# Optimization experiments

Hardware: AMD Instinct MI355X
Metric: run time of the kernel (lower is better)

The kernel has to match this reference:

```python
import jax, jax.numpy as jnp
import numpy as np

SEQ, BATCH, IN, HID, MID = 512, 64, 64, 512, 256


def setup_inputs() -> dict:
    key = jax.random.key(0)
    ks = jax.random.split(key, 8)
    concat_size = IN + 2 * HID  # 1088
    z_size = IN + MID  # 320
    sc = lambda n: 1.0 / np.sqrt(n)
    return {
        "x": jax.random.normal(ks[0], (SEQ, BATCH, IN), dtype=jnp.float32),
        "old_m": jax.random.normal(ks[1], (BATCH, HID), dtype=jnp.float32),
        "old_s": jnp.ones((BATCH, HID), dtype=jnp.float32),
        "W_z": jax.random.normal(ks[2], (MID, concat_size), dtype=jnp.float32) * sc(concat_size),
        "b_z": jnp.zeros((MID,), dtype=jnp.float32),
        "W_s": jax.random.normal(ks[3], (HID, z_size), dtype=jnp.float32) * sc(z_size),
        "b_s": jnp.zeros((HID,), dtype=jnp.float32),
        "W_m": jax.random.normal(ks[4], (HID, z_size), dtype=jnp.float32) * sc(z_size),
        "b_m": jnp.zeros((HID,), dtype=jnp.float32),
    }


def reference(x, old_m, old_s, W_z, b_z, W_s, b_s, W_m, b_m):
    def step(carry, x_t):
        m, s = carry  # [B, H] each
        z_inpt = jnp.concatenate([x_t, m, 1.0 / s], axis=-1)  # [B, IN+2H]
        z = jnp.concatenate([x_t, jnp.tanh(z_inpt @ W_z.T + b_z)], axis=-1)  # [B, IN+MID]
        new_s = s + jax.nn.sigmoid(z @ W_s.T + b_s)
        m_gate = jax.lax.stop_gradient(s / new_s)
        new_m = m_gate * m + (1.0 - m_gate) * jnp.tanh(z @ W_m.T + b_m)
        return (new_m, new_s), (new_m, new_s)

    _, (out_m, out_s) = jax.lax.scan(step, (old_m, old_s), x)
    return out_m, out_s
```

## Files before the change

### kernel.cpp

```cpp
#include <hip/hip_runtime.h>
#include <math.h>
#include <stdint.h>

#define SEQ    512
#define BATCH  64
#define IN_    64
#define HID    512
#define MID    256
#define CONCAT 1088
#define ZS     320
#define NW     4
#define QZ     64

typedef _Float16 h2t __attribute__((ext_vector_type(2)));

__device__ __forceinline__ float fdot2u(uint32_t a, uint32_t b, float c) {
    return __builtin_amdgcn_fdot2(__builtin_bit_cast(h2t, a),
                                  __builtin_bit_cast(h2t, b), c, false);
}
__device__ __forceinline__ uint32_t packrtn(float a, float b) {
    h2t h = { (_Float16)a, (_Float16)b };
    return __builtin_bit_cast(uint32_t, h);
}
template <int CTRL>
__device__ __forceinline__ float dpp_add(float v) {
    int o = __builtin_amdgcn_update_dpp(0, __builtin_bit_cast(int, v), CTRL, 0xF, 0xF, true);
    return v + __builtin_bit_cast(float, o);
}
template <int CTRL>
__device__ __forceinline__ float dpp_get(float v) {
    int o = __builtin_amdgcn_update_dpp(0, __builtin_bit_cast(int, v), CTRL, 0xF, 0xF, true);
    return __builtin_bit_cast(float, o);
}
__device__ __forceinline__ float red16(float v) {
    v = dpp_add<0xB1>(v);
    v = dpp_add<0x4E>(v);
    v = dpp_add<0x124>(v);
    v = dpp_add<0x128>(v);
    return v;
}
__device__ __forceinline__ int zidx(int k) { return (k / 34) * 36 + (k % 34); }

__device__ uint64_t g_px[(size_t)BATCH * 2 * NW * HID];

__global__ __launch_bounds__(512, 1)
void metamu8_kernel(const float* __restrict__ x,
                    const float* __restrict__ old_m,
                    const float* __restrict__ old_s,
                    const float* __restrict__ W_z,
                    const float* __restrict__ b_z,
                    const float* __restrict__ W_s,
                    const float* __restrict__ b_s,
                    const float* __restrict__ W_m,
                    const float* __restrict__ b_m,
                    float* __restrict__ out)
{
    const int bid = blockIdx.x;
    const int b   = bid & 63;
    const int w   = bid >> 6;
    const int tid = threadIdx.x;
    const int h   = tid;

    __shared__ __align__(16) uint32_t zin2[2][16 * 36];
    __shared__ __align__(16) uint32_t zvec2[2][40];

    const int g = tid >> 4, c = tid & 15;

    uint32_t wA0[34], wA1[34];
    {
        const float* p0 = W_z + (size_t)(QZ * w + 2 * g) * CONCAT + 68 * c;
        const float* p1 = p0 + CONCAT;
        #pragma unroll
        for (int i = 0; i < 34; ++i) {
            float2 a  = *reinterpret_cast<const float2*>(p0 + 2 * i);
            float2 bb = *reinterpret_cast<const float2*>(p1 + 2 * i);
            wA0[i] = packrtn(a.x, a.y);
            wA1[i] = packrtn(bb.x, bb.y);
        }
    }
    uint32_t wS[40], wM[40];
    {
        const float* ps = W_s + (size_t)h * ZS;
        const float* pm = W_m + (size_t)h * ZS;
        #pragma unroll
        for (int i = 0; i < 8; ++i) {
            float2 a  = *reinterpret_cast<const float2*>(ps + 16 * w + 2 * i);
            float2 bb = *reinterpret_cast<const float2*>(pm + 16 * w + 2 * i);
            wS[i] = packrtn(a.x, a.y);
            wM[i] = packrtn(bb.x, bb.y);
        }
        #pragma unroll
        for (int i = 0; i < 32; ++i) {
            float2 a  = *reinterpret_cast<const float2*>(ps + 64 + 64 * w + 2 * i);
            float2 bb = *reinterpret_cast<const float2*>(pm + 64 + 64 * w + 2 * i);
            wS[8 + i] = packrtn(a.x, a.y);
            wM[8 + i] = packrtn(bb.x, bb.y);
        }
    }
    const float bz0 = b_z[QZ * w + 2 * g], bz1 = b_z[QZ * w + 2 * g + 1];
    const float bsv = b_s[h], bmv = b_m[h];

    float sreg = old_s[b * HID + h];
    float mreg = old_m[b * HID + h];

    float2 xv = {0.f, 0.f};
    if (tid < 32) xv = *reinterpret_cast<const float2*>(x + (size_t)b * IN_ + 2 * tid);

    if (tid < 256) {
        float2 mv = *reinterpret_cast<const float2*>(old_m + b * HID + 2 * tid);
        zin2[0][zidx(32 + tid)] = packrtn(mv.x, mv.y);
    } else {
        const int j = tid - 256;
        float2 sv = *reinterpret_cast<const float2*>(old_s + b * HID + 2 * j);
        zin2[0][zidx(288 + j)] = packrtn(__builtin_amdgcn_rcpf(sv.x),
                                         __builtin_amdgcn_rcpf(sv.y));
    }
    if (tid < 32) zin2[0][zidx(tid)] = packrtn(xv.x, xv.y);
    if (tid >= 8 * w && tid < 8 * w + 8) zvec2[0][tid - 8 * w] = packrtn(xv.x, xv.y);
    __syncthreads();

    float* __restrict__ out_m = out;
    float* __restrict__ out_s = out + (size_t)SEQ * BATCH * HID;

    for (int t = 0; t < SEQ; ++t) {
        const int par = t & 1;
        const int np  = par ^ 1;
        const uint64_t want = (uint64_t)(t + 1);

        {
            uint32_t zf[34];
            const uint32_t* zc = &zin2[par][c * 36];
            #pragma unroll
            for (int i = 0; i < 8; ++i) {
                uint4 v = *reinterpret_cast<const uint4*>(zc + 4 * i);
                zf[4 * i] = v.x; zf[4 * i + 1] = v.y; zf[4 * i + 2] = v.z; zf[4 * i + 3] = v.w;
            }
            { uint2 v = *reinterpret_cast<const uint2*>(zc + 32); zf[32] = v.x; zf[33] = v.y; }
            float a0 = 0.f, a1 = 0.f;
            #pragma unroll
            for (int i = 0; i < 34; ++i) {
                a0 = fdot2u(wA0[i], zf[i], a0);
                a1 = fdot2u(wA1[i], zf[i], a1);
            }
            a0 = red16(a0);
            a1 = red16(a1);
            if (c == 0)
                zvec2[par][8 + g] = packrtn(tanhf(a0 + bz0), tanhf(a1 + bz1));
        }
        __syncthreads();

        float as = 0.f, am = 0.f;
        {
            uint32_t zg[40];
            #pragma unroll
            for (int i = 0; i < 10; ++i) {
                uint4 v = *reinterpret_cast<const uint4*>(&zvec2[par][4 * i]);
                zg[4 * i] = v.x; zg[4 * i + 1] = v.y; zg[4 * i + 2] = v.z; zg[4 * i + 3] = v.w;
            }
            #pragma unroll
            for (int i = 0; i < 40; ++i) {
                as = fdot2u(wS[i], zg[i], as);
                am = fdot2u(wM[i], zg[i], am);
            }
        }
        __hip_atomic_store(&g_px[(((size_t)b * 2 + par) * NW + w) * HID + h],
                           (want << 32) | (uint64_t)packrtn(as, am),
                           __ATOMIC_RELAXED, __HIP_MEMORY_SCOPE_AGENT);
        asm volatile("s_waitcnt vmcnt(0)" ::: "memory");

        if (tid < 32 && t + 1 < SEQ)
            xv = *reinterpret_cast<const float2*>(
                x + ((size_t)(t + 1) * BATCH + b) * IN_ + 2 * tid);

        {
            const size_t base = ((size_t)b * 2 + par) * NW;
            const uint64_t* s0 = &g_px[(base + ((w + 1) & 3)) * HID + h];
            const uint64_t* s1 = &g_px[(base + ((w + 2) & 3)) * HID + h];
            const uint64_t* s2 = &g_px[(base + ((w + 3) & 3)) * HID + h];
            uint64_t p0 = __hip_atomic_load(s0, __ATOMIC_RELAXED, __HIP_MEMORY_SCOPE_AGENT);
            uint64_t p1 = __hip_atomic_load(s1, __ATOMIC_RELAXED, __HIP_MEMORY_SCOPE_AGENT);
            uint64_t p2 = __hip_atomic_load(s2, __ATOMIC_RELAXED, __HIP_MEMORY_SCOPE_AGENT);
            bool r0 = (p0 >> 32) == want;
            bool r1 = (p1 >> 32) == want;
            bool r2 = (p2 >> 32) == want;
            while (!(r0 && r1 && r2)) {
                __builtin_amdgcn_s_sleep(1);
                if (!r0) { p0 = __hip_atomic_load(s0, __ATOMIC_RELAXED, __HIP_MEMORY_SCOPE_AGENT); }
                if (!r1) { p1 = __hip_atomic_load(s1, __ATOMIC_RELAXED, __HIP_MEMORY_SCOPE_AGENT); }
                if (!r2) { p2 = __hip_atomic_load(s2, __ATOMIC_RELAXED, __HIP_MEMORY_SCOPE_AGENT); }
                r0 = (p0 >> 32) == want;
                r1 = (p1 >> 32) == want;
                r2 = (p2 >> 32) == want;
            }
            h2t h0 = __builtin_bit_cast(h2t, (uint32_t)p0);
            h2t h1 = __builtin_bit_cast(h2t, (uint32_t)p1);
            h2t h2 = __builtin_bit_cast(h2t, (uint32_t)p2);
            as += (float)h0.x + (float)h1.x + (float)h2.x;
            am += (float)h0.y + (float)h1.y + (float)h2.y;
        }

        const float sig  = 1.f / (1.f + expf(-(as + bsv)));
        const float ns   = sreg + sig;
        const float gate = sreg / ns;
        const float nm   = gate * mreg + (1.f - gate) * tanhf(am + bmv);
        const float inv  = __builtin_amdgcn_rcpf(ns);
        sreg = ns; mreg = nm;

        if ((h >> 7) == w) {
            const size_t o = ((size_t)t * BATCH + b) * HID + h;
            out_m[o] = nm;
            out_s[o] = ns;
        }

        const float nm_n  = dpp_get<0xB1>(nm);
        const float inv_n = dpp_get<0xB1>(inv);
        if ((tid & 1) == 0) {
            zin2[np][zidx(32 + (tid >> 1))]  = packrtn(nm, nm_n);
            zin2[np][zidx(288 + (tid >> 1))] = packrtn(inv, inv_n);
        }
        if (t + 1 < SEQ) {
            if (tid < 32) zin2[np][zidx(tid)] = packrtn(xv.x, xv.y);
            if (tid >= 8 * w && tid < 8 * w + 8)
                zvec2[np][tid - 8 * w] = packrtn(xv.x, xv.y);
        }
        __syncthreads();
    }
}

extern "C" void kernel_launch(void* const* d_in, const int* in_sizes, int n_in,
                              void* d_out, int out_size, void* d_ws, size_t ws_size,
                              hipStream_t stream) {
    const float* x     = (const float*)d_in[0];
    const float* old_m = (const float*)d_in[1];
    const float* old_s = (const float*)d_in[2];
    const float* W_z   = (const float*)d_in[3];
    const float* b_z   = (const float*)d_in[4];
    const float* W_s   = (const float*)d_in[5];
    const float* b_s   = (const float*)d_in[6];
    const float* W_m   = (const float*)d_in[7];
    const float* b_m   = (const float*)d_in[8];

    metamu8_kernel<<<dim3(BATCH * NW), dim3(512), 0, stream>>>(
        x, old_m, old_s, W_z, b_z, W_s, b_s, W_m, b_m, (float*)d_out);
}
```

Measured before the change: 1.148 ms.

## Repartition recurrent matvecs across lanes and use fast exp/rcp activations

The W_z matvec now gives each 32-lane group four output rows with 17-element slices per lane, finished by a DPP plus ds_swizzle reduction. The W_s/W_m matvec splits each hidden unit's dot product across a lane pair, which halves the serial fdot2 chain per thread, and closes it with a DPP add. The padded LDS layout for z input changes to match the new slicing. tanhf/expf/division are replaced with v_exp_f32 and rcp based approximations to shorten the per-step critical path, at some cost in accuracy.

```diff
diff --git a/kernel.cpp b/kernel.cpp
--- a/kernel.cpp
+++ b/kernel.cpp
@@ -11,6 +11,7 @@
 #define ZS     320
 #define NW     4
 #define QZ     64
+#define L2E    1.4426950408889634f
 
 typedef _Float16 h2t __attribute__((ext_vector_type(2)));
 
@@ -39,12 +40,28 @@
     v = dpp_add<0x128>(v);
     return v;
 }
-__device__ __forceinline__ int zidx(int k) { return (k / 34) * 36 + (k % 34); }
+__device__ __forceinline__ float sw_add16(float v) {
+    int o = __builtin_amdgcn_ds_swizzle(__builtin_bit_cast(int, v), 0x401F);
+    return v + __builtin_bit_cast(float, o);
+}
+__device__ __forceinline__ float fexp2(float x) {
+    float r;
+    asm("v_exp_f32 %0, %1" : "=v"(r) : "v"(x));
+    return r;
+}
+__device__ __forceinline__ float frcp(float x) { return __builtin_amdgcn_rcpf(x); }
+__device__ __forceinline__ float fsigmoid(float x) {
+    return frcp(1.f + fexp2(-x * L2E));
+}
+__device__ __forceinline__ float ftanh(float x) {
+    return 1.f - 2.f * frcp(fexp2(x * (2.f * L2E)) + 1.f);
+}
+__device__ __forceinline__ int zidx(int k) { return (k / 17) * 20 + (k % 17); }
 
 __device__ uint64_t g_px[(size_t)BATCH * 2 * NW * HID];
 
 __global__ __launch_bounds__(512, 1)
-void metamu8_kernel(const float* __restrict__ x,
+void metamu9_kernel(const float* __restrict__ x,
                     const float* __restrict__ old_m,
                     const float* __restrict__ old_s,
                     const float* __restrict__ W_z,
@@ -61,43 +78,53 @@
     const int tid = threadIdx.x;
     const int h   = tid;
 
-    __shared__ __align__(16) uint32_t zin2[2][16 * 36];
+    __shared__ __align__(16) uint32_t zin2[2][32 * 20];
     __shared__ __align__(16) uint32_t zvec2[2][40];
 
-    const int g = tid >> 4, c = tid & 15;
-
-    uint32_t wA0[34], wA1[34];
+    const int g2 = tid >> 5, c2 = tid & 31;
+    const int l  = tid & 1;
+
+    uint32_t wA[4][17];
+    #pragma unroll
+    for (int r = 0; r < 4; ++r) {
+        const float* p = W_z + (size_t)(QZ * w + 4 * g2 + r) * CONCAT + 34 * c2;
+        #pragma unroll
+        for (int i = 0; i < 17; ++i) {
+            float2 a = *reinterpret_cast<const float2*>(p + 2 * i);
+            wA[r][i] = packrtn(a.x, a.y);
+        }
+    }
+    uint32_t wS0[20], wM0[20], wS1[20], wM1[20];
     {
-        const float* p0 = W_z + (size_t)(QZ * w + 2 * g) * CONCAT + 68 * c;
-        const float* p1 = p0 + CONCAT;
+        const int h0 = tid & ~1, h1 = tid | 1;
+        const float* ps0 = W_s + (size_t)h0 * ZS;
+        const float* pm0 = W_m + (size_t)h0 * ZS;
+        const float* ps1 = W_s + (size_t)h1 * ZS;
+        const float* pm1 = W_m + (size_t)h1 * ZS;
         #pragma unroll
-        for (int i = 0; i < 34; ++i) {
-            float2 a  = *reinterpret_cast<const float2*>(p0 + 2 * i);
-            float2 bb = *reinterpret_cast<const float2*>(p1 + 2 * i);
-            wA0[i] = packrtn(a.x, a.y);
-            wA1[i] = packrtn(bb.x, bb.y);
-        }
-    }
-    uint32_t wS[40], wM[40];
-    {
-        const float* ps = W_s + (size_t)h * ZS;
-        const float* pm = W_m + (size_t)h * ZS;
+        for (int i = 0; i < 4; ++i) {
+            const int o = 16 * w + 8 * l + 2 * i;
+            float2 a0 = *reinterpret_cast<const float2*>(ps0 + o);
+            float2 b0 = *reinterpret_cast<const float2*>(pm0 + o);
+            float2 a1 = *reinterpret_cast<const float2*>(ps1 + o);
+            float2 b1 = *reinterpret_cast<const float2*>(pm1 + o);
+            wS0[i] = packrtn(a0.x, a0.y); wM0[i] = packrtn(b0.x, b0.y);
+            wS1[i] = packrtn(a1.x, a1.y); wM1[i] = packrtn(b1.x, b1.y);
+        }
         #pragma unroll
-        for (int i = 0; i < 8; ++i) {
-            float2 a  = *reinterpret_cast<const float2*>(ps + 16 * w + 2 * i);
-            float2 bb = *reinterpret_cast<const float2*>(pm + 16 * w + 2 * i);
-            wS[i] = packrtn(a.x, a.y);
-            wM[i] = packrtn(bb.x, bb.y);
-        }
-        #pragma unroll
-        for (int i = 0; i < 32; ++i) {
-            float2 a  = *reinterpret_cast<const float2*>(ps + 64 + 64 * w + 2 * i);
-            float2 bb = *reinterpret_cast<const float2*>(pm + 64 + 64 * w + 2 * i);
-            wS[8 + i] = packrtn(a.x, a.y);
-            wM[8 + i] = packrtn(bb.x, bb.y);
-        }
-    }
-    const float bz0 = b_z[QZ * w + 2 * g], bz1 = b_z[QZ * w + 2 * g + 1];
+        for (int i = 0; i < 16; ++i) {
+            const int o = 64 + 64 * w + 32 * l + 2 * i;
+            float2 a0 = *reinterpret_cast<const float2*>(ps0 + o);
+            float2 b0 = *reinterpret_cast<const float2*>(pm0 + o);
+            float2 a1 = *reinterpret_cast<const float2*>(ps1 + o);
+            float2 b1 = *reinterpret_cast<const float2*>(pm1 + o);
+            wS0[4 + i] = packrtn(a0.x, a0.y); wM0[4 + i] = packrtn(b0.x, b0.y);
+            wS1[4 + i] = packrtn(a1.x, a1.y); wM1[4 + i] = packrtn(b1.x, b1.y);
+        }
+    }
+    float bz[4];
+    #pragma unroll
+    for (int r = 0; r < 4; ++r) bz[r] = b_z[QZ * w + 4 * g2 + r];
     const float bsv = b_s[h], bmv = b_m[h];
 
     float sreg = old_s[b * HID + h];
@@ -112,8 +139,7 @@
     } else {
         const int j = tid - 256;
         float2 sv = *reinterpret_cast<const float2*>(old_s + b * HID + 2 * j);
-        zin2[0][zidx(288 + j)] = packrtn(__builtin_amdgcn_rcpf(sv.x),
-                                         __builtin_amdgcn_rcpf(sv.y));
+        zin2[0][zidx(288 + j)] = packrtn(frcp(sv.x), frcp(sv.y));
     }
     if (tid < 32) zin2[0][zidx(tid)] = packrtn(xv.x, xv.y);
     if (tid >= 8 * w && tid < 8 * w + 8) zvec2[0][tid - 8 * w] = packrtn(xv.x, xv.y);
@@ -128,40 +154,60 @@
         const uint64_t want = (uint64_t)(t + 1);
 
         {
-            uint32_t zf[34];
-            const uint32_t* zc = &zin2[par][c * 36];
-            #pragma unroll
-            for (int i = 0; i < 8; ++i) {
+            uint32_t zf[17];
+            const uint32_t* zc = &zin2[par][c2 * 20];
+            #pragma unroll
+            for (int i = 0; i < 4; ++i) {
                 uint4 v = *reinterpret_cast<const uint4*>(zc + 4 * i);
                 zf[4 * i] = v.x; zf[4 * i + 1] = v.y; zf[4 * i + 2] = v.z; zf[4 * i + 3] = v.w;
             }
-            { uint2 v = *reinterpret_cast<const uint2*>(zc + 32); zf[32] = v.x; zf[33] = v.y; }
-            float a0 = 0.f, a1 = 0.f;
-            #pragma unroll
-            for (int i = 0; i < 34; ++i) {
-                a0 = fdot2u(wA0[i], zf[i], a0);
-                a1 = fdot2u(wA1[i], zf[i], a1);
-            }
-            a0 = red16(a0);
-            a1 = red16(a1);
-            if (c == 0)
-                zvec2[par][8 + g] = packrtn(tanhf(a0 + bz0), tanhf(a1 + bz1));
+            zf[16] = zc[16];
+            float a0 = 0.f, a1 = 0.f, a2 = 0.f, a3 = 0.f;
+            #pragma unroll
+            for (int i = 0; i < 17; ++i) {
+                a0 = fdot2u(wA[0][i], zf[i], a0);
+                a1 = fdot2u(wA[1][i], zf[i], a1);
+                a2 = fdot2u(wA[2][i], zf[i], a2);
+                a3 = fdot2u(wA[3][i], zf[i], a3);
+            }
+            a0 = sw_add16(red16(a0));
+            a1 = sw_add16(red16(a1));
+            a2 = sw_add16(red16(a2));
+            a3 = sw_add16(red16(a3));
+            if (c2 == 0) {
+                zvec2[par][8 + 2 * g2]     = packrtn(ftanh(a0 + bz[0]), ftanh(a1 + bz[1]));
+                zvec2[par][8 + 2 * g2 + 1] = packrtn(ftanh(a2 + bz[2]), ftanh(a3 + bz[3]));
+            }
         }
         __syncthreads();
 
-        float as = 0.f, am = 0.f;
+        float as, am;
         {
-            uint32_t zg[40];
-            #pragma unroll
-            for (int i = 0; i < 10; ++i) {
-                uint4 v = *reinterpret_cast<const uint4*>(&zvec2[par][4 * i]);
-                zg[4 * i] = v.x; zg[4 * i + 1] = v.y; zg[4 * i + 2] = v.z; zg[4 * i + 3] = v.w;
-            }
-            #pragma unroll
-            for (int i = 0; i < 40; ++i) {
-                as = fdot2u(wS[i], zg[i], as);
-                am = fdot2u(wM[i], zg[i], am);
-            }
+            uint32_t zg[20];
+            {
+                uint4 v = *reinterpret_cast<const uint4*>(&zvec2[par][4 * l]);
+                zg[0] = v.x; zg[1] = v.y; zg[2] = v.z; zg[3] = v.w;
+            }
+            const uint32_t* zc2 = &zvec2[par][8 + 16 * l];
+            #pragma unroll
+            for (int i = 0; i < 4; ++i) {
+                uint4 v = *reinterpret_cast<const uint4*>(zc2 + 4 * i);
+                zg[4 + 4 * i] = v.x; zg[5 + 4 * i] = v.y; zg[6 + 4 * i] = v.z; zg[7 + 4 * i] = v.w;
+            }
+            float as0 = 0.f, am0 = 0.f, as1 = 0.f, am1 = 0.f;
+            #pragma unroll
+            for (int i = 0; i < 20; ++i) {
+                as0 = fdot2u(wS0[i], zg[i], as0);
+                am0 = fdot2u(wM0[i], zg[i], am0);
+                as1 = fdot2u(wS1[i], zg[i], as1);
+                am1 = fdot2u(wM1[i], zg[i], am1);
+            }
+            as0 = dpp_add<0xB1>(as0);
+            am0 = dpp_add<0xB1>(am0);
+            as1 = dpp_add<0xB1>(as1);
+            am1 = dpp_add<0xB1>(am1);
+            as = l ? as1 : as0;
+            am = l ? am1 : am0;
         }
         __hip_atomic_store(&g_px[(((size_t)b * 2 + par) * NW + w) * HID + h],
                            (want << 32) | (uint64_t)packrtn(as, am),
@@ -199,11 +245,11 @@
             am += (float)h0.y + (float)h1.y + (float)h2.y;
         }
 
-        const float sig  = 1.f / (1.f + expf(-(as + bsv)));
+        const float sig  = fsigmoid(as + bsv);
         const float ns   = sreg + sig;
-        const float gate = sreg / ns;
-        const float nm   = gate * mreg + (1.f - gate) * tanhf(am + bmv);
-        const float inv  = __builtin_amdgcn_rcpf(ns);
+        const float inv  = frcp(ns);
+        const float gate = sreg * inv;
+        const float nm   = gate * mreg + (1.f - gate) * ftanh(am + bmv);
         sreg = ns; mreg = nm;
 
         if ((h >> 7) == w) {
@@ -240,6 +286,6 @@
     const float* W_m   = (const float*)d_in[7];
     const float* b_m   = (const float*)d_in[8];
 
-    metamu8_kernel<<<dim3(BATCH * NW), dim3(512), 0, stream>>>(
+    metamu9_kernel<<<dim3(BATCH * NW), dim3(512), 0, stream>>>(
         x, old_m, old_s, W_z, b_z, W_s, b_s, W_m, b_m, (float*)d_out);
 }
```

Result: faster. 1.041 ms (-9.3%).
